# Optimization experiments

Measured on AMD Instinct MI355X. Metric: run time of the kernel, lower is better.

Reference implementation:

```python
import jax, jax.numpy as jnp
import numpy as np

N_NODES = 100000
N_EDGES = 3200000
N_FEAT = 64
N_CLASS = 16


def setup_inputs() -> dict:
    key = jax.random.key(0)
    k1, k2, k3, k4 = jax.random.split(key, 4)
    x = jax.random.normal(k1, (N_NODES, N_FEAT), dtype=jnp.float32)
    weight = jax.random.normal(k2, (N_CLASS, N_FEAT), dtype=jnp.float32) * 0.1
    bias = jax.random.normal(k3, (N_CLASS,), dtype=jnp.float32) * 0.1
    edge_index = jax.random.randint(k4, (2, N_EDGES), 0, N_NODES, dtype=jnp.int64)
    return {"x": x, "weight": weight, "bias": bias, "edge_index": edge_index, "k": 3}


def reference(x, weight, bias, edge_index, k):
    # SGConv: x' = (D^-1/2 (A + I) D^-1/2)^K X, then Linear, then log_softmax.
    n = x.shape[0]
    loop = jnp.arange(n, dtype=edge_index.dtype)
    src = jnp.concatenate([edge_index[0], loop])  # add self-loops
    dst = jnp.concatenate([edge_index[1], loop])
    # gcn_norm: degree over destination nodes (edge weights all ones)
    deg = jax.ops.segment_sum(jnp.ones_like(src, dtype=x.dtype), dst, num_segments=n)
    dis = jnp.where(deg > 0, jax.lax.rsqrt(jnp.maximum(deg, 1)), 0.0).astype(x.dtype)
    norm = dis[src] * dis[dst]  # [E + N]
    for _ in range(k):
        # gather source features, scale, scatter-add to destinations
        x = jax.ops.segment_sum(x[src] * norm[:, None], dst, num_segments=n)
    logits = x @ weight.T + bias  # [N, C]
    return jax.nn.log_softmax(logits, axis=1)
```

## Files before the change

kernel.cpp:

```cpp
#include <hip/hip_runtime.h>
#include <hip/hip_fp16.h>

#define NFEAT 64
#define NCLS 16
#define MAXDEG 96
#define BSH 7
#define BSIZE 128
#define NBLK 512
#define NBMAX 1024
#define EPB 6272
#define CAP 4480
#define MINCP 32

__global__ void k_hist(const int* __restrict__ dst, int* __restrict__ G,
                       int nE, int epb, int nb) {
    __shared__ int h[NBMAX];
    int j = blockIdx.x;
    for (int t = threadIdx.x; t < nb; t += blockDim.x) h[t] = 0;
    __syncthreads();
    int e0 = j * epb, e1 = min(e0 + epb, nE);
    for (int e = e0 + threadIdx.x; e < e1; e += blockDim.x)
        atomicAdd(&h[dst[e] >> BSH], 1);
    __syncthreads();
    for (int t = threadIdx.x; t < nb; t += blockDim.x)
        G[(size_t)j * nb + t] = h[t];
}

__global__ void k_gscan(const int* __restrict__ G, int* __restrict__ btot,
                        int* __restrict__ BASE, int nb) {
    __shared__ int wt[NBLK / 64];
    int b = blockIdx.x, t = threadIdx.x;
    int lane = t & 63, wv = t >> 6;
    int v = G[(size_t)t * nb + b];
    int s = v;
#pragma unroll
    for (int off = 1; off < 64; off <<= 1) {
        int u = __shfl_up(s, off);
        if (lane >= off) s += u;
    }
    if (lane == 63) wt[wv] = s;
    __syncthreads();
    int pre = 0, tot = 0;
#pragma unroll
    for (int w = 0; w < NBLK / 64; ++w) {
        if (w < wv) pre += wt[w];
        tot += wt[w];
    }
    if (t == 0) btot[b] = tot;
    BASE[(size_t)t * nb + b] = b * CAP + pre + s - v;
}

__global__ void k_binsort(const int* __restrict__ src, const int* __restrict__ dst,
                          const int* __restrict__ G, const int* __restrict__ BASE,
                          int* __restrict__ pairs, int nE, int epb, int nb) {
    __shared__ int ebuf[EPB];
    __shared__ int gbuf[EPB];
    __shared__ int loc[NBMAX];
    __shared__ int gb[NBMAX];
    __shared__ int wt[NBMAX / 64];
    int j = blockIdx.x, tid = threadIdx.x;
    int lane = tid & 63, wv = tid >> 6;
    int v = (tid < nb) ? G[(size_t)j * nb + tid] : 0;
    int s = v;
#pragma unroll
    for (int off = 1; off < 64; off <<= 1) {
        int u = __shfl_up(s, off);
        if (lane >= off) s += u;
    }
    if (lane == 63) wt[wv] = s;
    __syncthreads();
    int pre = 0;
#pragma unroll
    for (int w = 0; w < NBMAX / 64; ++w) if (w < wv) pre += wt[w];
    int excl = pre + s - v;
    loc[tid] = excl;
    if (tid < nb) gb[tid] = BASE[(size_t)j * nb + tid] - excl;
    __syncthreads();
    int e0 = j * epb, e1 = min(e0 + epb, nE);
    for (int e = e0 + tid; e < e1; e += blockDim.x) {
        int d = dst[e], ssrc = src[e];
        int b = d >> BSH;
        int p = atomicAdd(&loc[b], 1);
        ebuf[p] = ((d & (BSIZE - 1)) << 17) | ssrc;
        gbuf[p] = gb[b] + p;
    }
    __syncthreads();
    int m = e1 - e0;
    for (int p = tid; p < m; p += blockDim.x)
        pairs[gbuf[p]] = ebuf[p];
}

__global__ void k_csr(const int* __restrict__ pairs, const int* __restrict__ btot,
                      int* __restrict__ ssortP, int4* __restrict__ aux,
                      float* __restrict__ dis, int n, int nb) {
    __shared__ int buf[BSIZE][MAXDEG];
    __shared__ int cnt[BSIZE];
    int b = blockIdx.x;
    for (int t = threadIdx.x; t < BSIZE; t += blockDim.x) cnt[t] = 0;
    __syncthreads();
    int e0 = b * CAP, e1 = e0 + btot[b];
    for (int e = e0 + threadIdx.x; e < e1; e += blockDim.x) {
        int pk = pairs[e];
        int s = pk & 0x1FFFF;
        int ld = ((unsigned)pk) >> 17;
        int p = atomicAdd(&cnt[ld], 1);
        if (p < MAXDEG) buf[ld][p] = s;
    }
    __syncthreads();
    for (int idx = threadIdx.x; idx < BSIZE * MAXDEG; idx += blockDim.x) {
        int ld = idx / MAXDEG, p = idx - ld * MAXDEG;
        int node = (b << BSH) + ld;
        int c = min(cnt[ld], MAXDEG - 1);
        int cp = (c + 1 + 15) & ~15;
        if (cp < MINCP) cp = MINCP;
        if (node < n && p < cp) {
            int val = (p < c) ? buf[ld][p] : ((p == c) ? node : n);
            ssortP[(size_t)node * MAXDEG + p] = val;
        }
    }
    int node = (b << BSH) + threadIdx.x;
    if (threadIdx.x < BSIZE && node < n) {
        int c = min(cnt[threadIdx.x], MAXDEG - 1);
        float d = (float)(c + 1);
        float ds = rsqrtf(d);
        dis[node] = ds;
        aux[node] = make_int4(c + 1, __float_as_int(ds * ds), __float_as_int(sqrtf(d)), 0);
    }
}

__global__ void k_lin0(const float* __restrict__ x, const float* __restrict__ w,
                       const float* __restrict__ dis, __half* __restrict__ za,
                       __half* __restrict__ zb, int n) {
    __shared__ float4 ws4[NCLS * 17];
    for (int i = threadIdx.x; i < NCLS * 16; i += blockDim.x) {
        int c = i >> 4, j = i & 15;
        ws4[c * 17 + j] = ((const float4*)w)[i];
    }
    __syncthreads();
    int t = blockIdx.x * blockDim.x + threadIdx.x;
    int node = t >> 2;
    if (node > n) return;
    int q = t & 3;
    if (node == n) {
        ((int2*)(za + (size_t)n * NCLS))[q] = make_int2(0, 0);
        ((int2*)(zb + (size_t)n * NCLS))[q] = make_int2(0, 0);
        return;
    }
    const float4* xr = (const float4*)(x + (size_t)node * NFEAT);
    const float4* wq = &ws4[(q << 2) * 17];
    float a0 = 0.f, a1 = 0.f, a2 = 0.f, a3 = 0.f;
#pragma unroll
    for (int j = 0; j < 16; ++j) {
        float4 v  = xr[j];
        float4 w0 = wq[j];
        float4 w1 = wq[17 + j];
        float4 w2 = wq[34 + j];
        float4 w3 = wq[51 + j];
        a0 += v.x * w0.x + v.y * w0.y + v.z * w0.z + v.w * w0.w;
        a1 += v.x * w1.x + v.y * w1.y + v.z * w1.z + v.w * w1.w;
        a2 += v.x * w2.x + v.y * w2.y + v.z * w2.z + v.w * w2.w;
        a3 += v.x * w3.x + v.y * w3.y + v.z * w3.z + v.w * w3.w;
    }
    float d = dis[node];
    __half2 h01 = __floats2half2_rn(a0 * d, a1 * d);
    __half2 h23 = __floats2half2_rn(a2 * d, a3 * d);
    __half2* o = (__half2*)(za + (size_t)node * NCLS) + (q << 1);
    o[0] = h01;
    o[1] = h23;
}

__device__ inline void acc8(int4 v, float* a) {
    __half2 t; float2 f;
    *(int*)&t = v.x; f = __half22float2(t); a[0] += f.x; a[1] += f.y;
    *(int*)&t = v.y; f = __half22float2(t); a[2] += f.x; a[3] += f.y;
    *(int*)&t = v.z; f = __half22float2(t); a[4] += f.x; a[5] += f.y;
    *(int*)&t = v.w; f = __half22float2(t); a[6] += f.x; a[7] += f.y;
}
__device__ inline int pkh2(float x, float y) {
    __half2 r = __floats2half2_rn(x, y);
    return *(int*)&r;
}

template <bool FINAL>
__global__ void __launch_bounds__(256, 8)
k_prop16(const __half* __restrict__ zin, __half* __restrict__ zout,
         const int4* __restrict__ aux, const int* __restrict__ ssortP,
         const float* __restrict__ bias, float* __restrict__ out, int n) {
    int t = blockIdx.x * blockDim.x + threadIdx.x;
    int wid = t >> 6;
    int lane = threadIdx.x & 63;
    int g2 = lane >> 4;
    int e3 = (lane >> 1) & 7;
    int h8 = (lane & 1) << 3;
    int node = wid * 4 + g2;
    bool valid = node < n;
    int nd = valid ? node : (n - 1);
    int4 ax = aux[nd];
    const int* row = ssortP + (size_t)nd * MAXDEG + 2 * e3;
    int2 r0 = *(const int2*)(row);
    int2 r1 = *(const int2*)(row + 16);
    int dg = ax.x;
    if (dg > MAXDEG) dg = MAXDEG;
    int2 r2 = make_int2(n, n), r3 = r2, r4 = r2, r5 = r2;
    if (dg > 32) r2 = *(const int2*)(row + 32);
    if (dg > 48) r3 = *(const int2*)(row + 48);
    if (dg > 64) r4 = *(const int2*)(row + 64);
    if (dg > 80) r5 = *(const int2*)(row + 80);
    float a[8] = {0.f, 0.f, 0.f, 0.f, 0.f, 0.f, 0.f, 0.f};
#define GATH2(rr) { \
        int4 vA = *(const int4*)(zin + (size_t)(rr).x * NCLS + h8); \
        int4 vB = *(const int4*)(zin + (size_t)(rr).y * NCLS + h8); \
        acc8(vA, a); acc8(vB, a); }
    GATH2(r0);
    GATH2(r1);
    if (dg > 32) GATH2(r2);
    if (dg > 48) GATH2(r3);
    if (dg > 64) GATH2(r4);
    if (dg > 80) GATH2(r5);
#undef GATH2
#pragma unroll
    for (int i = 0; i < 8; ++i) {
        a[i] += __shfl_xor(a[i], 2);
        a[i] += __shfl_xor(a[i], 4);
        a[i] += __shfl_xor(a[i], 8);
    }
    float d2 = __int_as_float(ax.y);
    if (!FINAL) {
        if (valid && e3 == 0) {
            int4 o = make_int4(pkh2(a[0] * d2, a[1] * d2), pkh2(a[2] * d2, a[3] * d2),
                               pkh2(a[4] * d2, a[5] * d2), pkh2(a[6] * d2, a[7] * d2));
            *(int4*)(zout + (size_t)node * NCLS + h8) = o;
        }
    } else {
        float rd = __int_as_float(ax.z);
        float sc = d2 * rd;
        int hq = h8 >> 2;
        float4 b0 = ((const float4*)bias)[hq];
        float4 b1 = ((const float4*)bias)[hq + 1];
        float lg[8];
        lg[0] = a[0] * sc + b0.x; lg[1] = a[1] * sc + b0.y;
        lg[2] = a[2] * sc + b0.z; lg[3] = a[3] * sc + b0.w;
        lg[4] = a[4] * sc + b1.x; lg[5] = a[5] * sc + b1.y;
        lg[6] = a[6] * sc + b1.z; lg[7] = a[7] * sc + b1.w;
        float m = fmaxf(fmaxf(fmaxf(lg[0], lg[1]), fmaxf(lg[2], lg[3])),
                        fmaxf(fmaxf(lg[4], lg[5]), fmaxf(lg[6], lg[7])));
        m = fmaxf(m, __shfl_xor(m, 1));
        float s = 0.f;
#pragma unroll
        for (int i = 0; i < 8; ++i) s += expf(lg[i] - m);
        s += __shfl_xor(s, 1);
        float lse = m + logf(s);
        if (valid && e3 == 0) {
            float* orow = out + (size_t)node * NCLS + h8;
            ((float4*)orow)[0] = make_float4(lg[0] - lse, lg[1] - lse, lg[2] - lse, lg[3] - lse);
            ((float4*)orow)[1] = make_float4(lg[4] - lse, lg[5] - lse, lg[6] - lse, lg[7] - lse);
        }
    }
}

extern "C" void kernel_launch(void* const* d_in, const int* in_sizes, int n_in,
                              void* d_out, int out_size, void* d_ws, size_t ws_size,
                              hipStream_t stream) {
    const float* x    = (const float*)d_in[0];
    const float* w    = (const float*)d_in[1];
    const float* bias = (const float*)d_in[2];
    const int*   ei   = (const int*)d_in[3];

    int n  = in_sizes[0] / NFEAT;
    int nE = in_sizes[3] / 2;
    const int* src = ei;
    const int* dst = ei + nE;

    int nb  = (n + BSIZE - 1) >> BSH;
    int epb = (nE + NBLK - 1) / NBLK;

    char* p = (char*)d_ws;
    auto alloc = [&](size_t bytes) { void* r = (void*)p; p += (bytes + 511) & ~511ULL; return r; };
    int*    ssortP = (int*)alloc((size_t)n * MAXDEG * 4);
    int*    pairs  = (int*)alloc((size_t)nb * CAP * 4);
    __half* za     = (__half*)alloc((size_t)(n + 1) * NCLS * 2);
    __half* zb     = (__half*)alloc((size_t)(n + 1) * NCLS * 2);
    int*    G      = (int*)alloc((size_t)NBLK * nb * 4);
    int*    BASE   = (int*)alloc((size_t)NBLK * nb * 4);
    int*    btot   = (int*)alloc((size_t)nb * 4);
    int4*   aux    = (int4*)G;
    float*  dis    = (float*)BASE;

    k_hist   <<<NBLK, 1024, 0, stream>>>(dst, G, nE, epb, nb);
    k_gscan  <<<nb, NBLK, 0, stream>>>(G, btot, BASE, nb);
    k_binsort<<<NBLK, 1024, 0, stream>>>(src, dst, G, BASE, pairs, nE, epb, nb);
    k_csr    <<<nb, 512, 0, stream>>>(pairs, btot, ssortP, aux, dis, n, nb);

    k_lin0<<<(4 * (n + 1) + 255) / 256, 256, 0, stream>>>(x, w, dis, za, zb, n);

    int nblk = (int)((((size_t)(n + 3) / 4) * 64 + 255) / 256);
    k_prop16<false><<<nblk, 256, 0, stream>>>(za, zb, aux, ssortP, bias, nullptr, n);
    k_prop16<false><<<nblk, 256, 0, stream>>>(zb, za, aux, ssortP, bias, nullptr, n);
    k_prop16<true> <<<nblk, 256, 0, stream>>>(za, nullptr, aux, ssortP, bias, (float*)d_out, n);
}
```

Baseline: 119.5 us.

## Drop global scan kernel; store per-block sorted segments and read them by offset table

Removes the k_gscan kernel and the scatter to globally bucketed positions. Each binsort block now writes its locally sorted edges contiguously with vectorized int4 stores and records per-bucket offsets in a transposed table. The CSR kernel then has each of its 512 threads read one source block's segment for its bucket. This saves a launch and replaces scattered stores with coalesced ones, but the CSR reads become short per-thread strided runs, and the data loads are less balanced across threads.

```diff
diff --git a/kernel.cpp b/kernel.cpp
--- a/kernel.cpp
+++ b/kernel.cpp
@@ -9,7 +9,6 @@
 #define NBLK 512
 #define NBMAX 1024
 #define EPB 6272
-#define CAP 4480
 #define MINCP 32
 
 __global__ void k_hist(const int* __restrict__ dst, int* __restrict__ G,
@@ -26,37 +25,11 @@
         G[(size_t)j * nb + t] = h[t];
 }
 
-__global__ void k_gscan(const int* __restrict__ G, int* __restrict__ btot,
-                        int* __restrict__ BASE, int nb) {
-    __shared__ int wt[NBLK / 64];
-    int b = blockIdx.x, t = threadIdx.x;
-    int lane = t & 63, wv = t >> 6;
-    int v = G[(size_t)t * nb + b];
-    int s = v;
-#pragma unroll
-    for (int off = 1; off < 64; off <<= 1) {
-        int u = __shfl_up(s, off);
-        if (lane >= off) s += u;
-    }
-    if (lane == 63) wt[wv] = s;
-    __syncthreads();
-    int pre = 0, tot = 0;
-#pragma unroll
-    for (int w = 0; w < NBLK / 64; ++w) {
-        if (w < wv) pre += wt[w];
-        tot += wt[w];
-    }
-    if (t == 0) btot[b] = tot;
-    BASE[(size_t)t * nb + b] = b * CAP + pre + s - v;
-}
-
 __global__ void k_binsort(const int* __restrict__ src, const int* __restrict__ dst,
-                          const int* __restrict__ G, const int* __restrict__ BASE,
+                          const int* __restrict__ G, int* __restrict__ LOCt,
                           int* __restrict__ pairs, int nE, int epb, int nb) {
     __shared__ int ebuf[EPB];
-    __shared__ int gbuf[EPB];
     __shared__ int loc[NBMAX];
-    __shared__ int gb[NBMAX];
     __shared__ int wt[NBMAX / 64];
     int j = blockIdx.x, tid = threadIdx.x;
     int lane = tid & 63, wv = tid >> 6;
@@ -74,40 +47,46 @@
     for (int w = 0; w < NBMAX / 64; ++w) if (w < wv) pre += wt[w];
     int excl = pre + s - v;
     loc[tid] = excl;
-    if (tid < nb) gb[tid] = BASE[(size_t)j * nb + tid] - excl;
-    __syncthreads();
     int e0 = j * epb, e1 = min(e0 + epb, nE);
+    int m = e1 - e0;
+    if (tid < nb) LOCt[(size_t)tid * NBLK + j] = excl;
+    if (tid == 0) LOCt[(size_t)nb * NBLK + j] = m;
+    __syncthreads();
     for (int e = e0 + tid; e < e1; e += blockDim.x) {
         int d = dst[e], ssrc = src[e];
         int b = d >> BSH;
         int p = atomicAdd(&loc[b], 1);
         ebuf[p] = ((d & (BSIZE - 1)) << 17) | ssrc;
-        gbuf[p] = gb[b] + p;
-    }
-    __syncthreads();
-    int m = e1 - e0;
-    for (int p = tid; p < m; p += blockDim.x)
-        pairs[gbuf[p]] = ebuf[p];
-}
-
-__global__ void k_csr(const int* __restrict__ pairs, const int* __restrict__ btot,
+    }
+    __syncthreads();
+    int* pj = pairs + (size_t)j * EPB;
+    int m4 = m & ~3;
+    for (int p = tid * 4; p < m4; p += blockDim.x * 4)
+        *(int4*)(pj + p) = *(const int4*)&ebuf[p];
+    for (int p = m4 + tid; p < m; p += blockDim.x)
+        pj[p] = ebuf[p];
+}
+
+__global__ void k_csr(const int* __restrict__ pairs, const int* __restrict__ LOCt,
                       int* __restrict__ ssortP, int4* __restrict__ aux,
                       float* __restrict__ dis, int n, int nb) {
     __shared__ int buf[BSIZE][MAXDEG];
     __shared__ int cnt[BSIZE];
-    int b = blockIdx.x;
-    for (int t = threadIdx.x; t < BSIZE; t += blockDim.x) cnt[t] = 0;
-    __syncthreads();
-    int e0 = b * CAP, e1 = e0 + btot[b];
-    for (int e = e0 + threadIdx.x; e < e1; e += blockDim.x) {
-        int pk = pairs[e];
+    int b = blockIdx.x, t = threadIdx.x;
+    for (int i = t; i < BSIZE; i += blockDim.x) cnt[i] = 0;
+    __syncthreads();
+    int s0 = LOCt[(size_t)b * NBLK + t];
+    int s1 = LOCt[(size_t)(b + 1) * NBLK + t];
+    const int* pj = pairs + (size_t)t * EPB;
+    for (int i = s0; i < s1; ++i) {
+        int pk = pj[i];
         int s = pk & 0x1FFFF;
         int ld = ((unsigned)pk) >> 17;
         int p = atomicAdd(&cnt[ld], 1);
         if (p < MAXDEG) buf[ld][p] = s;
     }
     __syncthreads();
-    for (int idx = threadIdx.x; idx < BSIZE * MAXDEG; idx += blockDim.x) {
+    for (int idx = t; idx < BSIZE * MAXDEG; idx += blockDim.x) {
         int ld = idx / MAXDEG, p = idx - ld * MAXDEG;
         int node = (b << BSH) + ld;
         int c = min(cnt[ld], MAXDEG - 1);
@@ -118,9 +97,9 @@
             ssortP[(size_t)node * MAXDEG + p] = val;
         }
     }
-    int node = (b << BSH) + threadIdx.x;
-    if (threadIdx.x < BSIZE && node < n) {
-        int c = min(cnt[threadIdx.x], MAXDEG - 1);
+    int node = (b << BSH) + t;
+    if (t < BSIZE && node < n) {
+        int c = min(cnt[t], MAXDEG - 1);
         float d = (float)(c + 1);
         float ds = rsqrtf(d);
         dis[node] = ds;
@@ -277,19 +256,17 @@
     char* p = (char*)d_ws;
     auto alloc = [&](size_t bytes) { void* r = (void*)p; p += (bytes + 511) & ~511ULL; return r; };
     int*    ssortP = (int*)alloc((size_t)n * MAXDEG * 4);
-    int*    pairs  = (int*)alloc((size_t)nb * CAP * 4);
+    int*    pairs  = (int*)alloc((size_t)NBLK * EPB * 4);
     __half* za     = (__half*)alloc((size_t)(n + 1) * NCLS * 2);
     __half* zb     = (__half*)alloc((size_t)(n + 1) * NCLS * 2);
     int*    G      = (int*)alloc((size_t)NBLK * nb * 4);
-    int*    BASE   = (int*)alloc((size_t)NBLK * nb * 4);
-    int*    btot   = (int*)alloc((size_t)nb * 4);
+    int*    LOCt   = (int*)alloc((size_t)(nb + 1) * NBLK * 4);
+    float*  dis    = (float*)alloc((size_t)n * 4);
     int4*   aux    = (int4*)G;
-    float*  dis    = (float*)BASE;
 
     k_hist   <<<NBLK, 1024, 0, stream>>>(dst, G, nE, epb, nb);
-    k_gscan  <<<nb, NBLK, 0, stream>>>(G, btot, BASE, nb);
-    k_binsort<<<NBLK, 1024, 0, stream>>>(src, dst, G, BASE, pairs, nE, epb, nb);
-    k_csr    <<<nb, 512, 0, stream>>>(pairs, btot, ssortP, aux, dis, n, nb);
+    k_binsort<<<NBLK, 1024, 0, stream>>>(src, dst, G, LOCt, pairs, nE, epb, nb);
+    k_csr    <<<nb, NBLK, 0, stream>>>(pairs, LOCt, ssortP, aux, dis, n, nb);
 
     k_lin0<<<(4 * (n + 1) + 255) / 256, 256, 0, stream>>>(x, w, dis, za, zb, n);
 
```

Measured after the change: 153.2 us. +28.1%, slower.
